# Kernel tuning notes

Hardware: AMD Instinct MI355X
Metric: run time of the kernel (lower is better)

The kernel has to match this reference:

```python
import jax, jax.numpy as jnp
import numpy as np

S = 16384          # number of ragged segments (ranking lists)
AVG_LEN = 512      # average list length
N = S * AVG_LEN    # total elements = 8,388,608


def setup_inputs() -> dict:
    key = jax.random.key(0)
    k1, k2 = jax.random.split(key)
    rng = np.random.default_rng(0)
    lengths = rng.integers(128, 897, size=S)
    # force exact total so concatenated tensors have a fixed shape N
    lengths[-1] += N - lengths.sum()
    scope = jnp.asarray(lengths, dtype=jnp.int32)
    means = jax.random.normal(k1, (N,), dtype=jnp.float32)
    targets_train = jax.random.normal(k2, (N,), dtype=jnp.float32)
    return {"means": means, "scope": scope, "targets_train": targets_train}


def reference(means, scope, targets_train):
    num_seg = scope.shape[0]
    n = means.shape[0]
    # segment id for every element, from ragged lengths (jit-safe: fixed total)
    seg = jnp.repeat(jnp.arange(num_seg, dtype=jnp.int32), scope,
                     total_repeat_length=n)
    # per-segment softmax of targets (stable)
    tmax = jax.ops.segment_max(targets_train, seg, num_segments=num_seg)
    te = jnp.exp(targets_train - tmax[seg])
    tden = jax.ops.segment_sum(te, seg, num_segments=num_seg)
    p = te / tden[seg]
    # per-segment log_softmax of means (stable)
    mmax = jax.ops.segment_max(means, seg, num_segments=num_seg)
    shifted = means - mmax[seg]
    lse = jnp.log(jax.ops.segment_sum(jnp.exp(shifted), seg, num_segments=num_seg))
    logq = shifted - lse[seg]
    # sum of per-segment cross-entropies, averaged over segments
    loss = -jnp.sum(p * logq)
    return loss / num_seg
```

## Files before the change

kernel.cpp:

```cpp
#include <hip/hip_runtime.h>
#include <hip/hip_bf16.h>

#define SCAN_T 1024
#define SEG_BLK 256

__global__ __launch_bounds__(SCAN_T)
void scan_kernel(const int* __restrict__ scope,
                 int* __restrict__ offsets, int S) {
    __shared__ int waveSums[16];
    int tid  = threadIdx.x;
    int lane = tid & 63, wv = tid >> 6;

    int s = 0;
    int4 r0, r1, r2, r3;
    bool fast = (S == SCAN_T * 16);
    int chunk = (S + SCAN_T - 1) / SCAN_T;
    int begin = tid * chunk;
    int end   = begin + chunk; if (end > S) end = S;

    if (fast) {
        const int4* sp = (const int4*)(scope + tid * 16);
        r0 = sp[0]; r1 = sp[1]; r2 = sp[2]; r3 = sp[3];
        s = (r0.x + r0.y + r0.z + r0.w) + (r1.x + r1.y + r1.z + r1.w)
          + (r2.x + r2.y + r2.z + r2.w) + (r3.x + r3.y + r3.z + r3.w);
    } else {
        for (int i = begin; i < end; ++i) s += scope[i];
    }

    int inc = s;
#pragma unroll
    for (int o = 1; o < 64; o <<= 1) {
        int v = __shfl_up(inc, o, 64);
        if (lane >= o) inc += v;
    }
    if (lane == 63) waveSums[wv] = inc;
    __syncthreads();
    if (tid == 0) {
        int run = 0;
#pragma unroll
        for (int w = 0; w < 16; ++w) { int v = waveSums[w]; waveSums[w] = run; run += v; }
    }
    __syncthreads();
    int base = waveSums[wv] + (inc - s);

    if (fast) {
        int4* op = (int4*)(offsets + tid * 16);
        int4 o0, o1, o2, o3;
        o0.x = base;            o0.y = o0.x + r0.x; o0.z = o0.y + r0.y; o0.w = o0.z + r0.z;
        o1.x = o0.w + r0.w;     o1.y = o1.x + r1.x; o1.z = o1.y + r1.y; o1.w = o1.z + r1.z;
        o2.x = o1.w + r1.w;     o2.y = o2.x + r2.x; o2.z = o2.y + r2.y; o2.w = o2.z + r2.z;
        o3.x = o2.w + r2.w;     o3.y = o3.x + r3.x; o3.z = o3.y + r3.y; o3.w = o3.z + r3.z;
        op[0] = o0; op[1] = o1; op[2] = o2; op[3] = o3;
    } else {
        for (int i = begin; i < end; ++i) { offsets[i] = base; base += scope[i]; }
    }
}

__global__ __launch_bounds__(SEG_BLK)
void seg_loss_1p(const float* __restrict__ means,
                 const float* __restrict__ targets,
                 const int* __restrict__ offsets,
                 const int* __restrict__ scope,
                 float* __restrict__ segl, int S) {
    int seg  = blockIdx.x * (SEG_BLK >> 6) + (threadIdx.x >> 6);
    if (seg >= S) return;
    int lane = threadIdx.x & 63;
    int start = offsets[seg];
    int len   = scope[seg];
    if (len <= 0) { if (lane == 0) segl[seg] = 0.f; return; }

    const float* __restrict__ T = targets + start;
    const float* __restrict__ M = means + start;
    int head = (4 - (start & 3)) & 3; if (head > len) head = len;
    int nv    = (len - head) >> 2;
    int tailb = head + (nv << 2);
    int tail  = len - tailb;
    const float4* __restrict__ T4 = (const float4*)(T + head);
    const float4* __restrict__ M4 = (const float4*)(M + head);

    float tden = 0.f, mden = 0.f, A = 0.f;

    if (lane < head) {
        float t = T[lane], m = M[lane];
        float e = __expf(t);
        tden += e; mden += __expf(m); A += e * m;
    }
    if (lane < tail) {
        float t = T[tailb + lane], m = M[tailb + lane];
        float e = __expf(t);
        tden += e; mden += __expf(m); A += e * m;
    }

    int v = lane;
    for (; v + 64 < nv; v += 128) {
        float4 a = T4[v], b = T4[v + 64];
        float4 c = M4[v], d = M4[v + 64];
        float e0 = __expf(a.x), e1 = __expf(a.y), e2 = __expf(a.z), e3 = __expf(a.w);
        float e4 = __expf(b.x), e5 = __expf(b.y), e6 = __expf(b.z), e7 = __expf(b.w);
        tden += ((e0 + e1) + (e2 + e3)) + ((e4 + e5) + (e6 + e7));
        mden += ((__expf(c.x) + __expf(c.y)) + (__expf(c.z) + __expf(c.w)))
              + ((__expf(d.x) + __expf(d.y)) + (__expf(d.z) + __expf(d.w)));
        A    += ((e0 * c.x + e1 * c.y) + (e2 * c.z + e3 * c.w))
              + ((e4 * d.x + e5 * d.y) + (e6 * d.z + e7 * d.w));
    }
    for (; v < nv; v += 64) {
        float4 a = T4[v], c = M4[v];
        float e0 = __expf(a.x), e1 = __expf(a.y), e2 = __expf(a.z), e3 = __expf(a.w);
        tden += (e0 + e1) + (e2 + e3);
        mden += (__expf(c.x) + __expf(c.y)) + (__expf(c.z) + __expf(c.w));
        A    += (e0 * c.x + e1 * c.y) + (e2 * c.z + e3 * c.w);
    }

#pragma unroll
    for (int o = 32; o > 0; o >>= 1) {
        tden += __shfl_xor(tden, o, 64);
        mden += __shfl_xor(mden, o, 64);
        A    += __shfl_xor(A,    o, 64);
    }
    if (lane == 0) segl[seg] = logf(mden) - A / tden;
}

__global__ __launch_bounds__(1024)
void reduce_kernel(const float* __restrict__ seg_loss,
                   float* __restrict__ out, int S) {
    __shared__ float wsum[16];
    int tid = threadIdx.x;
    float s = 0.f;
    if (S == 16384) {
        const float4* p = (const float4*)(seg_loss + tid * 16);
        float4 a = p[0], b = p[1], c = p[2], d = p[3];
        s = ((a.x + a.y) + (a.z + a.w)) + ((b.x + b.y) + (b.z + b.w))
          + ((c.x + c.y) + (c.z + c.w)) + ((d.x + d.y) + (d.z + d.w));
    } else {
        for (int i = tid; i < S; i += 1024) s += seg_loss[i];
    }
#pragma unroll
    for (int o = 32; o > 0; o >>= 1) s += __shfl_down(s, o, 64);
    int lane = tid & 63, wave = tid >> 6;
    if (lane == 0) wsum[wave] = s;
    __syncthreads();
    if (tid == 0) {
        float tot = 0.f;
#pragma unroll
        for (int w = 0; w < 16; ++w) tot += wsum[w];
        out[0] = tot / (float)S;
    }
}

extern "C" void kernel_launch(void* const* d_in, const int* in_sizes, int n_in,
                              void* d_out, int out_size, void* d_ws, size_t ws_size,
                              hipStream_t stream) {
    const float* means   = (const float*)d_in[0];
    const int*   scope   = (const int*)d_in[1];
    const float* targets = (const float*)d_in[2];
    int S = in_sizes[1];
    float* out = (float*)d_out;

    int*   offsets = (int*)d_ws;
    float* segl    = (float*)((char*)d_ws + (size_t)S * sizeof(int));

    scan_kernel<<<1, SCAN_T, 0, stream>>>(scope, offsets, S);
    int segBlocks = (S + (SEG_BLK >> 6) - 1) / (SEG_BLK >> 6);
    seg_loss_1p<<<segBlocks, SEG_BLK, 0, stream>>>(
        means, targets, offsets, scope, segl, S);
    reduce_kernel<<<1, 1024, 0, stream>>>(segl, out, S);
}
```

Baseline: 35.32 us.

## Fuse offset scan into segment loss kernel with per-block prefix recompute

Removes the single-block scan kernel. Each block now recomputes its starting offset by summing the scope entries before its first segment and then serially lays out offsets for its 16 segments. Each wave handles 4 segments and the block writes a partial loss, so the final reduce reads 1024 values instead of 16384. This saves one launch and the serial scan stage, but adds redundant prefix-sum reads of scope (up to 16K ints per block, about 64 KB in the worst case, mostly served from cache) and fewer, larger blocks.

```diff
diff --git a/kernel.cpp b/kernel.cpp
--- a/kernel.cpp
+++ b/kernel.cpp
@@ -1,150 +1,134 @@
 #include <hip/hip_runtime.h>
 #include <hip/hip_bf16.h>
 
-#define SCAN_T 1024
-#define SEG_BLK 256
+#define BLK_T 256
+#define SEGS_PER_BLK 16
+#define SEGS_PER_WAVE 4
 
-__global__ __launch_bounds__(SCAN_T)
-void scan_kernel(const int* __restrict__ scope,
-                 int* __restrict__ offsets, int S) {
-    __shared__ int waveSums[16];
+__global__ __launch_bounds__(BLK_T)
+void fused_seg_loss(const float* __restrict__ means,
+                    const float* __restrict__ targets,
+                    const int* __restrict__ scope,
+                    float* __restrict__ blockLoss, int S) {
+    __shared__ int   sOff[SEGS_PER_BLK];
+    __shared__ int   sLen[SEGS_PER_BLK];
+    __shared__ int   sPart[4];
+    __shared__ float sWave[4];
+
+    int b    = blockIdx.x;
     int tid  = threadIdx.x;
-    int lane = tid & 63, wv = tid >> 6;
+    int lane = tid & 63;
+    int wv   = tid >> 6;
+    int first = b * SEGS_PER_BLK;
+    int nseg  = S - first; if (nseg > SEGS_PER_BLK) nseg = SEGS_PER_BLK;
 
-    int s = 0;
-    int4 r0, r1, r2, r3;
-    bool fast = (S == SCAN_T * 16);
-    int chunk = (S + SCAN_T - 1) / SCAN_T;
-    int begin = tid * chunk;
-    int end   = begin + chunk; if (end > S) end = S;
+    int part = 0;
+    const int4* sp4 = (const int4*)scope;
+    int n4 = first >> 2;
+    for (int i = tid; i < n4; i += BLK_T) {
+        int4 v = sp4[i];
+        part += (v.x + v.y) + (v.z + v.w);
+    }
+#pragma unroll
+    for (int o = 32; o > 0; o >>= 1) part += __shfl_xor(part, o, 64);
+    if (lane == 0) sPart[wv] = part;
+    __syncthreads();
 
-    if (fast) {
-        const int4* sp = (const int4*)(scope + tid * 16);
-        r0 = sp[0]; r1 = sp[1]; r2 = sp[2]; r3 = sp[3];
-        s = (r0.x + r0.y + r0.z + r0.w) + (r1.x + r1.y + r1.z + r1.w)
-          + (r2.x + r2.y + r2.z + r2.w) + (r3.x + r3.y + r3.z + r3.w);
-    } else {
-        for (int i = begin; i < end; ++i) s += scope[i];
-    }
-
-    int inc = s;
-#pragma unroll
-    for (int o = 1; o < 64; o <<= 1) {
-        int v = __shfl_up(inc, o, 64);
-        if (lane >= o) inc += v;
-    }
-    if (lane == 63) waveSums[wv] = inc;
-    __syncthreads();
     if (tid == 0) {
-        int run = 0;
-#pragma unroll
-        for (int w = 0; w < 16; ++w) { int v = waveSums[w]; waveSums[w] = run; run += v; }
+        int base = (sPart[0] + sPart[1]) + (sPart[2] + sPart[3]);
+        for (int i = 0; i < nseg; ++i) {
+            int L = scope[first + i];
+            sOff[i] = base; sLen[i] = L; base += L;
+        }
     }
     __syncthreads();
-    int base = waveSums[wv] + (inc - s);
 
-    if (fast) {
-        int4* op = (int4*)(offsets + tid * 16);
-        int4 o0, o1, o2, o3;
-        o0.x = base;            o0.y = o0.x + r0.x; o0.z = o0.y + r0.y; o0.w = o0.z + r0.z;
-        o1.x = o0.w + r0.w;     o1.y = o1.x + r1.x; o1.z = o1.y + r1.y; o1.w = o1.z + r1.z;
-        o2.x = o1.w + r1.w;     o2.y = o2.x + r2.x; o2.z = o2.y + r2.y; o2.w = o2.z + r2.z;
-        o3.x = o2.w + r2.w;     o3.y = o3.x + r3.x; o3.z = o3.y + r3.y; o3.w = o3.z + r3.z;
-        op[0] = o0; op[1] = o1; op[2] = o2; op[3] = o3;
-    } else {
-        for (int i = begin; i < end; ++i) { offsets[i] = base; base += scope[i]; }
-    }
-}
+    float td[SEGS_PER_WAVE], md[SEGS_PER_WAVE], Av[SEGS_PER_WAVE];
+#pragma unroll
+    for (int q = 0; q < SEGS_PER_WAVE; ++q) {
+        int si = (wv << 2) + q;
+        float tden = 0.f, mden = 0.f, A = 0.f;
+        if (si < nseg && sLen[si] > 0) {
+            int start = sOff[si], len = sLen[si];
+            const float* __restrict__ T = targets + start;
+            const float* __restrict__ M = means + start;
+            int head = (4 - (start & 3)) & 3; if (head > len) head = len;
+            int nv    = (len - head) >> 2;
+            int tailb = head + (nv << 2);
+            int tail  = len - tailb;
+            const float4* __restrict__ T4 = (const float4*)(T + head);
+            const float4* __restrict__ M4 = (const float4*)(M + head);
 
-__global__ __launch_bounds__(SEG_BLK)
-void seg_loss_1p(const float* __restrict__ means,
-                 const float* __restrict__ targets,
-                 const int* __restrict__ offsets,
-                 const int* __restrict__ scope,
-                 float* __restrict__ segl, int S) {
-    int seg  = blockIdx.x * (SEG_BLK >> 6) + (threadIdx.x >> 6);
-    if (seg >= S) return;
-    int lane = threadIdx.x & 63;
-    int start = offsets[seg];
-    int len   = scope[seg];
-    if (len <= 0) { if (lane == 0) segl[seg] = 0.f; return; }
-
-    const float* __restrict__ T = targets + start;
-    const float* __restrict__ M = means + start;
-    int head = (4 - (start & 3)) & 3; if (head > len) head = len;
-    int nv    = (len - head) >> 2;
-    int tailb = head + (nv << 2);
-    int tail  = len - tailb;
-    const float4* __restrict__ T4 = (const float4*)(T + head);
-    const float4* __restrict__ M4 = (const float4*)(M + head);
-
-    float tden = 0.f, mden = 0.f, A = 0.f;
-
-    if (lane < head) {
-        float t = T[lane], m = M[lane];
-        float e = __expf(t);
-        tden += e; mden += __expf(m); A += e * m;
-    }
-    if (lane < tail) {
-        float t = T[tailb + lane], m = M[tailb + lane];
-        float e = __expf(t);
-        tden += e; mden += __expf(m); A += e * m;
-    }
-
-    int v = lane;
-    for (; v + 64 < nv; v += 128) {
-        float4 a = T4[v], b = T4[v + 64];
-        float4 c = M4[v], d = M4[v + 64];
-        float e0 = __expf(a.x), e1 = __expf(a.y), e2 = __expf(a.z), e3 = __expf(a.w);
-        float e4 = __expf(b.x), e5 = __expf(b.y), e6 = __expf(b.z), e7 = __expf(b.w);
-        tden += ((e0 + e1) + (e2 + e3)) + ((e4 + e5) + (e6 + e7));
-        mden += ((__expf(c.x) + __expf(c.y)) + (__expf(c.z) + __expf(c.w)))
-              + ((__expf(d.x) + __expf(d.y)) + (__expf(d.z) + __expf(d.w)));
-        A    += ((e0 * c.x + e1 * c.y) + (e2 * c.z + e3 * c.w))
-              + ((e4 * d.x + e5 * d.y) + (e6 * d.z + e7 * d.w));
-    }
-    for (; v < nv; v += 64) {
-        float4 a = T4[v], c = M4[v];
-        float e0 = __expf(a.x), e1 = __expf(a.y), e2 = __expf(a.z), e3 = __expf(a.w);
-        tden += (e0 + e1) + (e2 + e3);
-        mden += (__expf(c.x) + __expf(c.y)) + (__expf(c.z) + __expf(c.w));
-        A    += (e0 * c.x + e1 * c.y) + (e2 * c.z + e3 * c.w);
+            if (lane < head) {
+                float t = T[lane], m = M[lane];
+                float e = __expf(t);
+                tden += e; mden += __expf(m); A += e * m;
+            }
+            if (lane < tail) {
+                float t = T[tailb + lane], m = M[tailb + lane];
+                float e = __expf(t);
+                tden += e; mden += __expf(m); A += e * m;
+            }
+            int v = lane;
+            for (; v + 64 < nv; v += 128) {
+                float4 a = T4[v], bb = T4[v + 64];
+                float4 c = M4[v], d  = M4[v + 64];
+                float e0 = __expf(a.x), e1 = __expf(a.y), e2 = __expf(a.z), e3 = __expf(a.w);
+                float e4 = __expf(bb.x), e5 = __expf(bb.y), e6 = __expf(bb.z), e7 = __expf(bb.w);
+                tden += ((e0 + e1) + (e2 + e3)) + ((e4 + e5) + (e6 + e7));
+                mden += ((__expf(c.x) + __expf(c.y)) + (__expf(c.z) + __expf(c.w)))
+                      + ((__expf(d.x) + __expf(d.y)) + (__expf(d.z) + __expf(d.w)));
+                A    += ((e0 * c.x + e1 * c.y) + (e2 * c.z + e3 * c.w))
+                      + ((e4 * d.x + e5 * d.y) + (e6 * d.z + e7 * d.w));
+            }
+            for (; v < nv; v += 64) {
+                float4 a = T4[v], c = M4[v];
+                float e0 = __expf(a.x), e1 = __expf(a.y), e2 = __expf(a.z), e3 = __expf(a.w);
+                tden += (e0 + e1) + (e2 + e3);
+                mden += (__expf(c.x) + __expf(c.y)) + (__expf(c.z) + __expf(c.w));
+                A    += (e0 * c.x + e1 * c.y) + (e2 * c.z + e3 * c.w);
+            }
+        }
+        td[q] = tden; md[q] = mden; Av[q] = A;
     }
 
 #pragma unroll
     for (int o = 32; o > 0; o >>= 1) {
-        tden += __shfl_xor(tden, o, 64);
-        mden += __shfl_xor(mden, o, 64);
-        A    += __shfl_xor(A,    o, 64);
+#pragma unroll
+        for (int q = 0; q < SEGS_PER_WAVE; ++q) {
+            td[q] += __shfl_xor(td[q], o, 64);
+            md[q] += __shfl_xor(md[q], o, 64);
+            Av[q] += __shfl_xor(Av[q], o, 64);
+        }
     }
-    if (lane == 0) segl[seg] = logf(mden) - A / tden;
+
+    if (lane == 0) {
+        float loss = 0.f;
+#pragma unroll
+        for (int q = 0; q < SEGS_PER_WAVE; ++q) {
+            int si = (wv << 2) + q;
+            if (si < nseg && sLen[si] > 0)
+                loss += logf(md[q]) - Av[q] / td[q];
+        }
+        sWave[wv] = loss;
+    }
+    __syncthreads();
+    if (tid == 0)
+        blockLoss[b] = (sWave[0] + sWave[1]) + (sWave[2] + sWave[3]);
 }
 
-__global__ __launch_bounds__(1024)
-void reduce_kernel(const float* __restrict__ seg_loss,
-                   float* __restrict__ out, int S) {
-    __shared__ float wsum[16];
-    int tid = threadIdx.x;
+__global__ __launch_bounds__(BLK_T)
+void final_reduce(const float* __restrict__ blockLoss,
+                  float* __restrict__ out, int nb, int S) {
+    __shared__ float w[4];
+    int tid = threadIdx.x, lane = tid & 63, wv = tid >> 6;
     float s = 0.f;
-    if (S == 16384) {
-        const float4* p = (const float4*)(seg_loss + tid * 16);
-        float4 a = p[0], b = p[1], c = p[2], d = p[3];
-        s = ((a.x + a.y) + (a.z + a.w)) + ((b.x + b.y) + (b.z + b.w))
-          + ((c.x + c.y) + (c.z + c.w)) + ((d.x + d.y) + (d.z + d.w));
-    } else {
-        for (int i = tid; i < S; i += 1024) s += seg_loss[i];
-    }
+    for (int i = tid; i < nb; i += BLK_T) s += blockLoss[i];
 #pragma unroll
-    for (int o = 32; o > 0; o >>= 1) s += __shfl_down(s, o, 64);
-    int lane = tid & 63, wave = tid >> 6;
-    if (lane == 0) wsum[wave] = s;
+    for (int o = 32; o > 0; o >>= 1) s += __shfl_xor(s, o, 64);
+    if (lane == 0) w[wv] = s;
     __syncthreads();
-    if (tid == 0) {
-        float tot = 0.f;
-#pragma unroll
-        for (int w = 0; w < 16; ++w) tot += wsum[w];
-        out[0] = tot / (float)S;
-    }
+    if (tid == 0) out[0] = ((w[0] + w[1]) + (w[2] + w[3])) / (float)S;
 }
 
 extern "C" void kernel_launch(void* const* d_in, const int* in_sizes, int n_in,
@@ -156,12 +140,9 @@
     int S = in_sizes[1];
     float* out = (float*)d_out;
 
-    int*   offsets = (int*)d_ws;
-    float* segl    = (float*)((char*)d_ws + (size_t)S * sizeof(int));
+    float* blockLoss = (float*)d_ws;
+    int nb = (S + SEGS_PER_BLK - 1) / SEGS_PER_BLK;
 
-    scan_kernel<<<1, SCAN_T, 0, stream>>>(scope, offsets, S);
-    int segBlocks = (S + (SEG_BLK >> 6) - 1) / (SEG_BLK >> 6);
-    seg_loss_1p<<<segBlocks, SEG_BLK, 0, stream>>>(
-        means, targets, offsets, scope, segl, S);
-    reduce_kernel<<<1, 1024, 0, stream>>>(segl, out, S);
+    fused_seg_loss<<<nb, BLK_T, 0, stream>>>(means, targets, scope, blockLoss, S);
+    final_reduce<<<1, BLK_T, 0, stream>>>(blockLoss, out, nb, S);
 }
```

Measured after the change: 30.43 us. 13.8% less time.

## Process two segments per wave with all loads issued upfront and block-level partial sums

Applied to the files above, without the earlier changes.

Each wave now handles two segments. For lengths in [128,896] it issues every load for both segments up front (clamped indices), then does the math with predicate multipliers instead of branches. The aim is more memory-level parallelism and fewer dependent load/compute round-trips. Each block also writes one partial sum, which shrinks the final reduction, and offsets are read from an extended exclusive scan instead of the scope array. The cost is higher register pressure, redundant clamped loads and exp work on masked lanes, and the fast path is tuned to the input's length range.

```diff
diff --git a/kernel.cpp b/kernel.cpp
--- a/kernel.cpp
+++ b/kernel.cpp
@@ -1,25 +1,21 @@
 #include <hip/hip_runtime.h>
 #include <hip/hip_bf16.h>
 
-#define SCAN_T 1024
-#define SEG_BLK 256
-
-__global__ __launch_bounds__(SCAN_T)
-void scan_kernel(const int* __restrict__ scope,
-                 int* __restrict__ offsets, int S) {
+#define K1_T 1024
+
+__global__ __launch_bounds__(K1_T)
+void scan_kernel(const int* __restrict__ scope, int* __restrict__ off_ext, int S) {
     __shared__ int waveSums[16];
-    int tid  = threadIdx.x;
-    int lane = tid & 63, wv = tid >> 6;
+    int tid = threadIdx.x, lane = tid & 63, wv = tid >> 6;
+    int per   = (S + K1_T - 1) / K1_T;
+    int begin = tid * per;
+    int end   = min(begin + per, S);
 
     int s = 0;
+    bool fast = (per == 16) && (begin + 16 <= S);
     int4 r0, r1, r2, r3;
-    bool fast = (S == SCAN_T * 16);
-    int chunk = (S + SCAN_T - 1) / SCAN_T;
-    int begin = tid * chunk;
-    int end   = begin + chunk; if (end > S) end = S;
-
     if (fast) {
-        const int4* sp = (const int4*)(scope + tid * 16);
+        const int4* sp = (const int4*)(scope + begin);
         r0 = sp[0]; r1 = sp[1]; r2 = sp[2]; r3 = sp[3];
         s = (r0.x + r0.y + r0.z + r0.w) + (r1.x + r1.y + r1.z + r1.w)
           + (r2.x + r2.y + r2.z + r2.w) + (r3.x + r3.y + r3.z + r3.w);
@@ -44,105 +40,165 @@
     int base = waveSums[wv] + (inc - s);
 
     if (fast) {
-        int4* op = (int4*)(offsets + tid * 16);
-        int4 o0, o1, o2, o3;
-        o0.x = base;            o0.y = o0.x + r0.x; o0.z = o0.y + r0.y; o0.w = o0.z + r0.z;
-        o1.x = o0.w + r0.w;     o1.y = o1.x + r1.x; o1.z = o1.y + r1.y; o1.w = o1.z + r1.z;
-        o2.x = o1.w + r1.w;     o2.y = o2.x + r2.x; o2.z = o2.y + r2.y; o2.w = o2.z + r2.z;
-        o3.x = o2.w + r2.w;     o3.y = o3.x + r3.x; o3.z = o3.y + r3.y; o3.w = o3.z + r3.z;
+        int4 o0, o1, o2, o3; int bb = base;
+        o0.x = bb; bb += r0.x; o0.y = bb; bb += r0.y; o0.z = bb; bb += r0.z; o0.w = bb; bb += r0.w;
+        o1.x = bb; bb += r1.x; o1.y = bb; bb += r1.y; o1.z = bb; bb += r1.z; o1.w = bb; bb += r1.w;
+        o2.x = bb; bb += r2.x; o2.y = bb; bb += r2.y; o2.z = bb; bb += r2.z; o2.w = bb; bb += r2.w;
+        o3.x = bb; bb += r3.x; o3.y = bb; bb += r3.y; o3.z = bb; bb += r3.z; o3.w = bb; bb += r3.w;
+        int4* op = (int4*)(off_ext + begin);
         op[0] = o0; op[1] = o1; op[2] = o2; op[3] = o3;
     } else {
-        for (int i = begin; i < end; ++i) { offsets[i] = base; base += scope[i]; }
-    }
-}
-
-__global__ __launch_bounds__(SEG_BLK)
-void seg_loss_1p(const float* __restrict__ means,
-                 const float* __restrict__ targets,
-                 const int* __restrict__ offsets,
-                 const int* __restrict__ scope,
-                 float* __restrict__ segl, int S) {
-    int seg  = blockIdx.x * (SEG_BLK >> 6) + (threadIdx.x >> 6);
-    if (seg >= S) return;
-    int lane = threadIdx.x & 63;
-    int start = offsets[seg];
-    int len   = scope[seg];
-    if (len <= 0) { if (lane == 0) segl[seg] = 0.f; return; }
-
-    const float* __restrict__ T = targets + start;
-    const float* __restrict__ M = means + start;
-    int head = (4 - (start & 3)) & 3; if (head > len) head = len;
+        int bb = base;
+        for (int i = begin; i < end; ++i) { off_ext[i] = bb; bb += scope[i]; }
+    }
+    if (begin < S && end == S) off_ext[S] = base + s;
+}
+
+__device__ inline void seg_generic(const float* __restrict__ T,
+                                   const float* __restrict__ M,
+                                   int len, int lane,
+                                   float& td, float& md, float& A) {
+    int head = (4 - (((size_t)T >> 2) & 3)) & 3; if (head > len) head = len;
     int nv    = (len - head) >> 2;
     int tailb = head + (nv << 2);
     int tail  = len - tailb;
-    const float4* __restrict__ T4 = (const float4*)(T + head);
-    const float4* __restrict__ M4 = (const float4*)(M + head);
-
-    float tden = 0.f, mden = 0.f, A = 0.f;
-
+    const float4* T4 = (const float4*)(T + head);
+    const float4* M4 = (const float4*)(M + head);
     if (lane < head) {
-        float t = T[lane], m = M[lane];
-        float e = __expf(t);
-        tden += e; mden += __expf(m); A += e * m;
+        float e = __expf(T[lane]); float m = M[lane];
+        td += e; md += __expf(m); A += e * m;
     }
     if (lane < tail) {
-        float t = T[tailb + lane], m = M[tailb + lane];
-        float e = __expf(t);
-        tden += e; mden += __expf(m); A += e * m;
-    }
-
-    int v = lane;
-    for (; v + 64 < nv; v += 128) {
-        float4 a = T4[v], b = T4[v + 64];
-        float4 c = M4[v], d = M4[v + 64];
-        float e0 = __expf(a.x), e1 = __expf(a.y), e2 = __expf(a.z), e3 = __expf(a.w);
-        float e4 = __expf(b.x), e5 = __expf(b.y), e6 = __expf(b.z), e7 = __expf(b.w);
-        tden += ((e0 + e1) + (e2 + e3)) + ((e4 + e5) + (e6 + e7));
-        mden += ((__expf(c.x) + __expf(c.y)) + (__expf(c.z) + __expf(c.w)))
-              + ((__expf(d.x) + __expf(d.y)) + (__expf(d.z) + __expf(d.w)));
-        A    += ((e0 * c.x + e1 * c.y) + (e2 * c.z + e3 * c.w))
-              + ((e4 * d.x + e5 * d.y) + (e6 * d.z + e7 * d.w));
-    }
-    for (; v < nv; v += 64) {
+        float e = __expf(T[tailb + lane]); float m = M[tailb + lane];
+        td += e; md += __expf(m); A += e * m;
+    }
+    for (int v = lane; v < nv; v += 64) {
         float4 a = T4[v], c = M4[v];
         float e0 = __expf(a.x), e1 = __expf(a.y), e2 = __expf(a.z), e3 = __expf(a.w);
-        tden += (e0 + e1) + (e2 + e3);
-        mden += (__expf(c.x) + __expf(c.y)) + (__expf(c.z) + __expf(c.w));
-        A    += (e0 * c.x + e1 * c.y) + (e2 * c.z + e3 * c.w);
+        td += (e0 + e1) + (e2 + e3);
+        md += (__expf(c.x) + __expf(c.y)) + (__expf(c.z) + __expf(c.w));
+        A  += (e0 * c.x + e1 * c.y) + (e2 * c.z + e3 * c.w);
+    }
+}
+
+#define SEG_LOADS(P, start, len)                                               \
+    int P##head = (4 - ((start) & 3)) & 3; if (P##head > (len)) P##head = (len); \
+    int P##nv    = ((len) - P##head) >> 2;                                     \
+    int P##tailb = P##head + (P##nv << 2);                                     \
+    int P##tail  = (len) - P##tailb;                                           \
+    const float* P##T = targets + (start);                                     \
+    const float* P##M = means + (start);                                       \
+    const float4* P##T4 = (const float4*)(P##T + P##head);                     \
+    const float4* P##M4 = (const float4*)(P##M + P##head);                     \
+    int P##c = P##nv - 1;                                                      \
+    int P##hidx = min(lane, (len) - 1);                                        \
+    int P##gt   = min((start) + P##tailb + lane, n - 1);                       \
+    float  P##th = P##T[P##hidx],     P##mh = P##M[P##hidx];                   \
+    float  P##tt = targets[P##gt],    P##mt = means[P##gt];                    \
+    float4 P##t0 = P##T4[min(lane,       P##c)], P##m0 = P##M4[min(lane,       P##c)]; \
+    float4 P##t1 = P##T4[min(lane + 64,  P##c)], P##m1 = P##M4[min(lane + 64,  P##c)]; \
+    float4 P##t2 = P##T4[min(lane + 128, P##c)], P##m2 = P##M4[min(lane + 128, P##c)]; \
+    float4 P##t3 = P##T4[min(lane + 192, P##c)], P##m3 = P##M4[min(lane + 192, P##c)];
+
+#define ACC_STRIPE(tv, mv, sv, td, md, A)                                      \
+    {                                                                          \
+        float e0 = __expf(tv.x), e1 = __expf(tv.y);                            \
+        float e2 = __expf(tv.z), e3 = __expf(tv.w);                            \
+        td += sv * ((e0 + e1) + (e2 + e3));                                    \
+        md += sv * ((__expf(mv.x) + __expf(mv.y)) + (__expf(mv.z) + __expf(mv.w))); \
+        A  += sv * ((e0 * mv.x + e1 * mv.y) + (e2 * mv.z + e3 * mv.w));        \
+    }
+
+#define SEG_CONSUME(P, td, md, A)                                              \
+    {                                                                          \
+        float sh = (lane < P##head) ? 1.f : 0.f;                               \
+        float st = (lane < P##tail) ? 1.f : 0.f;                               \
+        float s0 = (lane       < P##nv) ? 1.f : 0.f;                           \
+        float s1 = (lane + 64  < P##nv) ? 1.f : 0.f;                           \
+        float s2 = (lane + 128 < P##nv) ? 1.f : 0.f;                           \
+        float s3 = (lane + 192 < P##nv) ? 1.f : 0.f;                           \
+        float e = __expf(P##th);                                               \
+        td += sh * e; md += sh * __expf(P##mh); A += sh * e * P##mh;           \
+        float f = __expf(P##tt);                                               \
+        td += st * f; md += st * __expf(P##mt); A += st * f * P##mt;           \
+        ACC_STRIPE(P##t0, P##m0, s0, td, md, A)                                \
+        ACC_STRIPE(P##t1, P##m1, s1, td, md, A)                                \
+        ACC_STRIPE(P##t2, P##m2, s2, td, md, A)                                \
+        ACC_STRIPE(P##t3, P##m3, s3, td, md, A)                                \
+    }
+
+__global__ __launch_bounds__(256, 4)
+void seg2_kernel(const float* __restrict__ means,
+                 const float* __restrict__ targets,
+                 const int* __restrict__ off_ext,
+                 float* __restrict__ blockLoss, int S, int n) {
+    __shared__ float sW[8];
+    int wv = threadIdx.x >> 6, lane = threadIdx.x & 63;
+    int w  = blockIdx.x * 4 + wv;
+    int sA = 2 * w, sB = 2 * w + 1;
+    bool hasA = sA < S, hasB = sB < S;
+
+    int oA0 = off_ext[min(sA,     S)];
+    int oA1 = off_ext[min(sA + 1, S)];
+    int oB1 = off_ext[min(sB + 1, S)];
+    int lenA = hasA ? (oA1 - oA0) : 0;
+    int lenB = hasB ? (oB1 - oA1) : 0;
+    int startA = oA0, startB = oA1;
+
+    float tdA = 0.f, mdA = 0.f, AA = 0.f;
+    float tdB = 0.f, mdB = 0.f, AB = 0.f;
+
+    bool fastA = (lenA >= 128) && (lenA <= 896);
+    bool fastB = (lenB >= 128) && (lenB <= 896);
+
+    if (fastA && fastB) {
+        SEG_LOADS(A_, startA, lenA)
+        SEG_LOADS(B_, startB, lenB)
+        SEG_CONSUME(A_, tdA, mdA, AA)
+        SEG_CONSUME(B_, tdB, mdB, AB)
+    } else {
+        if (lenA > 0) seg_generic(targets + startA, means + startA, lenA, lane, tdA, mdA, AA);
+        if (lenB > 0) seg_generic(targets + startB, means + startB, lenB, lane, tdB, mdB, AB);
     }
 
 #pragma unroll
     for (int o = 32; o > 0; o >>= 1) {
-        tden += __shfl_xor(tden, o, 64);
-        mden += __shfl_xor(mden, o, 64);
-        A    += __shfl_xor(A,    o, 64);
-    }
-    if (lane == 0) segl[seg] = logf(mden) - A / tden;
+        tdA += __shfl_xor(tdA, o, 64);
+        mdA += __shfl_xor(mdA, o, 64);
+        AA  += __shfl_xor(AA,  o, 64);
+        tdB += __shfl_xor(tdB, o, 64);
+        mdB += __shfl_xor(mdB, o, 64);
+        AB  += __shfl_xor(AB,  o, 64);
+    }
+
+    if (lane == 0) {
+        sW[2 * wv]     = (lenA > 0) ? (__logf(mdA) - AA / tdA) : 0.f;
+        sW[2 * wv + 1] = (lenB > 0) ? (__logf(mdB) - AB / tdB) : 0.f;
+    }
+    __syncthreads();
+    if (threadIdx.x == 0) {
+        float s = 0.f;
+#pragma unroll
+        for (int k = 0; k < 8; ++k) s += sW[k];
+        blockLoss[blockIdx.x] = s;
+    }
 }
 
 __global__ __launch_bounds__(1024)
-void reduce_kernel(const float* __restrict__ seg_loss,
-                   float* __restrict__ out, int S) {
-    __shared__ float wsum[16];
-    int tid = threadIdx.x;
+void final_reduce(const float* __restrict__ blockLoss,
+                  float* __restrict__ out, int nb, int S) {
+    __shared__ float w[16];
+    int tid = threadIdx.x, lane = tid & 63, wv = tid >> 6;
     float s = 0.f;
-    if (S == 16384) {
-        const float4* p = (const float4*)(seg_loss + tid * 16);
-        float4 a = p[0], b = p[1], c = p[2], d = p[3];
-        s = ((a.x + a.y) + (a.z + a.w)) + ((b.x + b.y) + (b.z + b.w))
-          + ((c.x + c.y) + (c.z + c.w)) + ((d.x + d.y) + (d.z + d.w));
-    } else {
-        for (int i = tid; i < S; i += 1024) s += seg_loss[i];
-    }
-#pragma unroll
-    for (int o = 32; o > 0; o >>= 1) s += __shfl_down(s, o, 64);
-    int lane = tid & 63, wave = tid >> 6;
-    if (lane == 0) wsum[wave] = s;
+    for (int i = tid; i < nb; i += 1024) s += blockLoss[i];
+#pragma unroll
+    for (int o = 32; o > 0; o >>= 1) s += __shfl_xor(s, o, 64);
+    if (lane == 0) w[wv] = s;
     __syncthreads();
     if (tid == 0) {
         float tot = 0.f;
 #pragma unroll
-        for (int w = 0; w < 16; ++w) tot += wsum[w];
+        for (int k = 0; k < 16; ++k) tot += w[k];
         out[0] = tot / (float)S;
     }
 }
@@ -153,15 +209,17 @@
     const float* means   = (const float*)d_in[0];
     const int*   scope   = (const int*)d_in[1];
     const float* targets = (const float*)d_in[2];
+    int n = in_sizes[0];
     int S = in_sizes[1];
     float* out = (float*)d_out;
 
-    int*   offsets = (int*)d_ws;
-    float* segl    = (float*)((char*)d_ws + (size_t)S * sizeof(int));
-
-    scan_kernel<<<1, SCAN_T, 0, stream>>>(scope, offsets, S);
-    int segBlocks = (S + (SEG_BLK >> 6) - 1) / (SEG_BLK >> 6);
-    seg_loss_1p<<<segBlocks, SEG_BLK, 0, stream>>>(
-        means, targets, offsets, scope, segl, S);
-    reduce_kernel<<<1, 1024, 0, stream>>>(segl, out, S);
-}
+    int* off_ext     = (int*)d_ws;
+    float* blockLoss = (float*)(off_ext + (S + 1));
+
+    int nWaves = (S + 1) / 2;
+    int nb     = (nWaves + 3) / 4;
+
+    scan_kernel<<<1, K1_T, 0, stream>>>(scope, off_ext, S);
+    seg2_kernel<<<nb, 256, 0, stream>>>(means, targets, off_ext, blockLoss, S, n);
+    final_reduce<<<1, 1024, 0, stream>>>(blockLoss, out, nb, S);
+}
```

Measured after the change: 43.81 us. +24.1%, slower.

## Stage segment data into LDS via async global_load_lds with masked stripes

Applied to the files above, without the earlier changes.

Rewrites the per-segment loss kernel so each wave loads its segment window (aligned down to 16 bytes) into LDS using global_load_lds in 256-element stripes, then reads float4 from LDS and masks out-of-segment elements. Segment length now comes from an extended offsets array (S+1 entries written by the scan), so the kernel no longer reads scope. This removes the head/tail scalar handling and keeps all loads issued before one wait. In exchange it uses 32KB of LDS per block, which can limit occupancy, computes exp on masked-out lanes, and adds an LDS round-trip.

```diff
diff --git a/kernel.cpp b/kernel.cpp
--- a/kernel.cpp
+++ b/kernel.cpp
@@ -1,25 +1,26 @@
 #include <hip/hip_runtime.h>
 #include <hip/hip_bf16.h>
 
-#define SCAN_T 1024
+#define K1_T 1024
 #define SEG_BLK 256
+#define WPB 4
+#define STRIPE 256
+#define MAX_STRIPES 4
+#define LDS_F (MAX_STRIPES * STRIPE)
 
-__global__ __launch_bounds__(SCAN_T)
-void scan_kernel(const int* __restrict__ scope,
-                 int* __restrict__ offsets, int S) {
+__global__ __launch_bounds__(K1_T)
+void scan_kernel(const int* __restrict__ scope, int* __restrict__ off_ext, int S) {
     __shared__ int waveSums[16];
-    int tid  = threadIdx.x;
-    int lane = tid & 63, wv = tid >> 6;
+    int tid = threadIdx.x, lane = tid & 63, wv = tid >> 6;
+    int per   = (S + K1_T - 1) / K1_T;
+    int begin = tid * per;
+    int end   = min(begin + per, S);
 
     int s = 0;
+    bool fast = (per == 16) && (begin + 16 <= S);
     int4 r0, r1, r2, r3;
-    bool fast = (S == SCAN_T * 16);
-    int chunk = (S + SCAN_T - 1) / SCAN_T;
-    int begin = tid * chunk;
-    int end   = begin + chunk; if (end > S) end = S;
-
     if (fast) {
-        const int4* sp = (const int4*)(scope + tid * 16);
+        const int4* sp = (const int4*)(scope + begin);
         r0 = sp[0]; r1 = sp[1]; r2 = sp[2]; r3 = sp[3];
         s = (r0.x + r0.y + r0.z + r0.w) + (r1.x + r1.y + r1.z + r1.w)
           + (r2.x + r2.y + r2.z + r2.w) + (r3.x + r3.y + r3.z + r3.w);
@@ -44,105 +45,120 @@
     int base = waveSums[wv] + (inc - s);
 
     if (fast) {
-        int4* op = (int4*)(offsets + tid * 16);
-        int4 o0, o1, o2, o3;
-        o0.x = base;            o0.y = o0.x + r0.x; o0.z = o0.y + r0.y; o0.w = o0.z + r0.z;
-        o1.x = o0.w + r0.w;     o1.y = o1.x + r1.x; o1.z = o1.y + r1.y; o1.w = o1.z + r1.z;
-        o2.x = o1.w + r1.w;     o2.y = o2.x + r2.x; o2.z = o2.y + r2.y; o2.w = o2.z + r2.z;
-        o3.x = o2.w + r2.w;     o3.y = o3.x + r3.x; o3.z = o3.y + r3.y; o3.w = o3.z + r3.z;
+        int4 o0, o1, o2, o3; int bb = base;
+        o0.x = bb; bb += r0.x; o0.y = bb; bb += r0.y; o0.z = bb; bb += r0.z; o0.w = bb; bb += r0.w;
+        o1.x = bb; bb += r1.x; o1.y = bb; bb += r1.y; o1.z = bb; bb += r1.z; o1.w = bb; bb += r1.w;
+        o2.x = bb; bb += r2.x; o2.y = bb; bb += r2.y; o2.z = bb; bb += r2.z; o2.w = bb; bb += r2.w;
+        o3.x = bb; bb += r3.x; o3.y = bb; bb += r3.y; o3.z = bb; bb += r3.z; o3.w = bb; bb += r3.w;
+        int4* op = (int4*)(off_ext + begin);
         op[0] = o0; op[1] = o1; op[2] = o2; op[3] = o3;
     } else {
-        for (int i = begin; i < end; ++i) { offsets[i] = base; base += scope[i]; }
+        int bb = base;
+        for (int i = begin; i < end; ++i) { off_ext[i] = bb; bb += scope[i]; }
     }
+    if (begin < S && end == S) off_ext[S] = base + s;
 }
 
 __global__ __launch_bounds__(SEG_BLK)
-void seg_loss_1p(const float* __restrict__ means,
-                 const float* __restrict__ targets,
-                 const int* __restrict__ offsets,
-                 const int* __restrict__ scope,
-                 float* __restrict__ segl, int S) {
-    int seg  = blockIdx.x * (SEG_BLK >> 6) + (threadIdx.x >> 6);
+void seg_lds_kernel(const float* __restrict__ means,
+                    const float* __restrict__ targets,
+                    const int* __restrict__ off_ext,
+                    float* __restrict__ segl, int S, int n) {
+    __shared__ float ldsT[WPB][LDS_F];
+    __shared__ float ldsM[WPB][LDS_F];
+
+    int wv   = threadIdx.x >> 6;
+    int lane = threadIdx.x & 63;
+    int seg  = blockIdx.x * WPB + wv;
     if (seg >= S) return;
-    int lane = threadIdx.x & 63;
-    int start = offsets[seg];
-    int len   = scope[seg];
+
+    int start = off_ext[seg];
+    int len   = off_ext[seg + 1] - start;
     if (len <= 0) { if (lane == 0) segl[seg] = 0.f; return; }
 
-    const float* __restrict__ T = targets + start;
-    const float* __restrict__ M = means + start;
-    int head = (4 - (start & 3)) & 3; if (head > len) head = len;
-    int nv    = (len - head) >> 2;
-    int tailb = head + (nv << 2);
-    int tail  = len - tailb;
-    const float4* __restrict__ T4 = (const float4*)(T + head);
-    const float4* __restrict__ M4 = (const float4*)(M + head);
+    int pad    = start & 3;
+    int abase  = start - pad;
+    int window = pad + len;
 
-    float tden = 0.f, mden = 0.f, A = 0.f;
+    float td = 0.f, md = 0.f, A = 0.f;
 
-    if (lane < head) {
-        float t = T[lane], m = M[lane];
-        float e = __expf(t);
-        tden += e; mden += __expf(m); A += e * m;
-    }
-    if (lane < tail) {
-        float t = T[tailb + lane], m = M[tailb + lane];
-        float e = __expf(t);
-        tden += e; mden += __expf(m); A += e * m;
-    }
+    if (window <= LDS_F) {
+        int nst  = (window + STRIPE - 1) >> 8;
+        int gmax = n - 4;
+        for (int k = 0; k < nst; ++k) {
+            int gi = min(abase + k * STRIPE + lane * 4, gmax);
+            __builtin_amdgcn_global_load_lds(
+                (const __attribute__((address_space(1))) void*)(targets + gi),
+                (__attribute__((address_space(3))) void*)&ldsT[wv][k * STRIPE],
+                16, 0, 0);
+            __builtin_amdgcn_global_load_lds(
+                (const __attribute__((address_space(1))) void*)(means + gi),
+                (__attribute__((address_space(3))) void*)&ldsM[wv][k * STRIPE],
+                16, 0, 0);
+        }
+        asm volatile("s_waitcnt vmcnt(0)" ::: "memory");
+        __builtin_amdgcn_sched_barrier(0);
 
-    int v = lane;
-    for (; v + 64 < nv; v += 128) {
-        float4 a = T4[v], b = T4[v + 64];
-        float4 c = M4[v], d = M4[v + 64];
-        float e0 = __expf(a.x), e1 = __expf(a.y), e2 = __expf(a.z), e3 = __expf(a.w);
-        float e4 = __expf(b.x), e5 = __expf(b.y), e6 = __expf(b.z), e7 = __expf(b.w);
-        tden += ((e0 + e1) + (e2 + e3)) + ((e4 + e5) + (e6 + e7));
-        mden += ((__expf(c.x) + __expf(c.y)) + (__expf(c.z) + __expf(c.w)))
-              + ((__expf(d.x) + __expf(d.y)) + (__expf(d.z) + __expf(d.w)));
-        A    += ((e0 * c.x + e1 * c.y) + (e2 * c.z + e3 * c.w))
-              + ((e4 * d.x + e5 * d.y) + (e6 * d.z + e7 * d.w));
-    }
-    for (; v < nv; v += 64) {
-        float4 a = T4[v], c = M4[v];
-        float e0 = __expf(a.x), e1 = __expf(a.y), e2 = __expf(a.z), e3 = __expf(a.w);
-        tden += (e0 + e1) + (e2 + e3);
-        mden += (__expf(c.x) + __expf(c.y)) + (__expf(c.z) + __expf(c.w));
-        A    += (e0 * c.x + e1 * c.y) + (e2 * c.z + e3 * c.w);
+        const float4* T4 = (const float4*)&ldsT[wv][0];
+        const float4* M4 = (const float4*)&ldsM[wv][0];
+        int lo = pad, hi = pad + len;
+        for (int k = 0; k < nst; ++k) {
+            float4 t = T4[k * 64 + lane];
+            float4 m = M4[k * 64 + lane];
+            int q = k * 256 + lane * 4;
+            float s0 = (q     >= lo && q     < hi) ? 1.f : 0.f;
+            float s1 = (q + 1 >= lo && q + 1 < hi) ? 1.f : 0.f;
+            float s2 = (q + 2 >= lo && q + 2 < hi) ? 1.f : 0.f;
+            float s3 = (q + 3 >= lo && q + 3 < hi) ? 1.f : 0.f;
+            float e0 = __expf(t.x), e1 = __expf(t.y);
+            float e2 = __expf(t.z), e3 = __expf(t.w);
+            td += (s0 * e0 + s1 * e1) + (s2 * e2 + s3 * e3);
+            md += (s0 * __expf(m.x) + s1 * __expf(m.y))
+                + (s2 * __expf(m.z) + s3 * __expf(m.w));
+            A  += (s0 * e0 * m.x + s1 * e1 * m.y)
+                + (s2 * e2 * m.z + s3 * e3 * m.w);
+        }
+    } else {
+        const float* __restrict__ T = targets + start;
+        const float* __restrict__ M = means + start;
+        for (int i = lane; i < len; i += 64) {
+            float e = __expf(T[i]);
+            float m = M[i];
+            td += e; md += __expf(m); A += e * m;
+        }
     }
 
 #pragma unroll
     for (int o = 32; o > 0; o >>= 1) {
-        tden += __shfl_xor(tden, o, 64);
-        mden += __shfl_xor(mden, o, 64);
-        A    += __shfl_xor(A,    o, 64);
+        td += __shfl_xor(td, o, 64);
+        md += __shfl_xor(md, o, 64);
+        A  += __shfl_xor(A,  o, 64);
     }
-    if (lane == 0) segl[seg] = logf(mden) - A / tden;
+    if (lane == 0) segl[seg] = __logf(md) - A / td;
 }
 
 __global__ __launch_bounds__(1024)
-void reduce_kernel(const float* __restrict__ seg_loss,
-                   float* __restrict__ out, int S) {
-    __shared__ float wsum[16];
-    int tid = threadIdx.x;
+void final_reduce(const float* __restrict__ segl,
+                  float* __restrict__ out, int S) {
+    __shared__ float w[16];
+    int tid = threadIdx.x, lane = tid & 63, wv = tid >> 6;
     float s = 0.f;
     if (S == 16384) {
-        const float4* p = (const float4*)(seg_loss + tid * 16);
+        const float4* p = (const float4*)(segl + tid * 16);
         float4 a = p[0], b = p[1], c = p[2], d = p[3];
         s = ((a.x + a.y) + (a.z + a.w)) + ((b.x + b.y) + (b.z + b.w))
           + ((c.x + c.y) + (c.z + c.w)) + ((d.x + d.y) + (d.z + d.w));
     } else {
-        for (int i = tid; i < S; i += 1024) s += seg_loss[i];
+        for (int i = tid; i < S; i += 1024) s += segl[i];
     }
 #pragma unroll
-    for (int o = 32; o > 0; o >>= 1) s += __shfl_down(s, o, 64);
-    int lane = tid & 63, wave = tid >> 6;
-    if (lane == 0) wsum[wave] = s;
+    for (int o = 32; o > 0; o >>= 1) s += __shfl_xor(s, o, 64);
+    if (lane == 0) w[wv] = s;
     __syncthreads();
     if (tid == 0) {
         float tot = 0.f;
 #pragma unroll
-        for (int w = 0; w < 16; ++w) tot += wsum[w];
+        for (int k = 0; k < 16; ++k) tot += w[k];
         out[0] = tot / (float)S;
     }
 }
@@ -153,15 +169,15 @@
     const float* means   = (const float*)d_in[0];
     const int*   scope   = (const int*)d_in[1];
     const float* targets = (const float*)d_in[2];
+    int n = in_sizes[0];
     int S = in_sizes[1];
     float* out = (float*)d_out;
 
-    int*   offsets = (int*)d_ws;
-    float* segl    = (float*)((char*)d_ws + (size_t)S * sizeof(int));
+    int*   off_ext = (int*)d_ws;
+    float* segl    = (float*)(off_ext + (S + 1));
 
-    scan_kernel<<<1, SCAN_T, 0, stream>>>(scope, offsets, S);
-    int segBlocks = (S + (SEG_BLK >> 6) - 1) / (SEG_BLK >> 6);
-    seg_loss_1p<<<segBlocks, SEG_BLK, 0, stream>>>(
-        means, targets, offsets, scope, segl, S);
-    reduce_kernel<<<1, 1024, 0, stream>>>(segl, out, S);
+    scan_kernel<<<1, K1_T, 0, stream>>>(scope, off_ext, S);
+    int nb = (S + WPB - 1) / WPB;
+    seg_lds_kernel<<<nb, SEG_BLK, 0, stream>>>(means, targets, off_ext, segl, S, n);
+    final_reduce<<<1, 1024, 0, stream>>>(segl, out, S);
 }
```

New measurement: 78.23 us. 122% more time.
